# Kernel tuning notes

Hardware: AMD Instinct MI355X
Metric: run time of the kernel (lower is better)

## Reference

```python
import jax, jax.numpy as jnp
import numpy as np

PAD, BOS, EOS, UNK = 0, 1, 2, 3
B, S, V, D, L = 256, 512, 50000, 256, 128

def setup_inputs() -> dict:
    key = jax.random.key(0)
    ks = jax.random.split(key, 12)
    vocab_tensor = jax.random.randint(ks[0], (B, S), 4, V)
    parent_idx = jax.random.randint(ks[1], (B, S), 0, S)
    pbond = jax.random.randint(ks[2], (B, S), 0, 4)
    bond = jax.random.randint(ks[3], (B, S), 0, 4)
    patom = jax.random.randint(ks[4], (B, S), 0, 16)
    atom = jax.random.randint(ks[5], (B, S), 0, 16)
    btype = jax.random.randint(ks[6], (B, S), 0, 4)
    order_tensor = jnp.stack([parent_idx, pbond, bond, patom, atom, btype], axis=-1)
    lengths = jax.random.randint(ks[7], (B,), 1, S + 1)
    mask_tensor = jnp.arange(S)[None, :] < lengths[:, None]  # ragged prefix masks
    eps = jax.random.normal(ks[8], (B, L), dtype=jnp.float32)
    sc = 1.0 / np.sqrt(D)
    emb = jax.random.normal(ks[9], (V, D), dtype=jnp.float32) * sc
    Wm = jax.random.normal(ks[10], (D, L), dtype=jnp.float32) * sc
    Wv = jax.random.normal(ks[11], (D, L), dtype=jnp.float32) * sc
    Wlin = jax.random.normal(jax.random.fold_in(key, 20), (L, D), dtype=jnp.float32) / np.sqrt(L)
    Wout = jax.random.normal(jax.random.fold_in(key, 21), (D, D), dtype=jnp.float32) * sc
    return {
        'vocab_tensor': vocab_tensor, 'order_tensor': order_tensor, 'mask_tensor': mask_tensor,
        'eps': eps, 'emb': emb, 'Wm': Wm, 'bm': jnp.zeros((L,), jnp.float32),
        'Wv': Wv, 'bv': jnp.zeros((L,), jnp.float32), 'Wlin': Wlin,
        'blin': jnp.zeros((D,), jnp.float32), 'Wout': Wout, 'bout': jnp.zeros((D,), jnp.float32),
    }

def _forward(vocab_tensor, order_tensor, mask_tensor, eps, emb, Wm, bm, Wv, bv, Wlin, blin, Wout, bout):
    # --- mask bond-pos columns (torch.where assignments, vectorized) ---
    # (columns 1 and 2 set to -1 where masked; kept implicitly via vt/pad handling)
    # --- calc_chem_z path: masked vocab, parent gather, edge one-hot ---
    vt = jnp.where(mask_tensor, vocab_tensor, PAD)                      # [B,S]
    vocab_emb = emb[vt]                                                 # [B,S,D]
    oi = order_tensor[..., 0]
    oi = jnp.where(oi == -1, BOS, oi)
    parent = jnp.where(mask_tensor, jnp.take_along_axis(vt, oi, axis=1), PAD)
    parent = parent.at[:, 0].set(BOS)
    parent_emb = emb[parent]                                            # [B,S,D]
    idx = jnp.clip(order_tensor[..., 5] - 1, -1, None)
    edge_type = jnp.where((idx >= 0)[..., None],
                          jax.nn.one_hot(jnp.clip(idx, 0), 3, dtype=jnp.float32), 0.0)  # [B,S,3]
    # pooling stand-in for (undefined) StructureEncoder -> [B,D]
    m = mask_tensor[..., None].astype(jnp.float32)
    enc = ((vocab_emb + parent_emb) * m).sum(1) / jnp.maximum(m.sum(1), 1.0)
    enc = enc * (1.0 + 0.0 * edge_type.sum())  # keep edge_type in graph
    # --- LatentSampler ---
    mean = enc @ Wm + bm
    log_var = enc @ Wv + bv
    z = mean + eps * jnp.exp(0.5 * log_var)
    memory = z @ Wlin + blin                                            # [B,D]
    # --- vectorized bos/eos/pad sequence assembly (the hot loop in torch) ---
    inp = jnp.concatenate([jnp.full((B, 1), BOS, vocab_tensor.dtype), vocab_tensor], axis=1)  # [B,S+1]
    mask_ex = jnp.concatenate([jnp.ones((B, 1), bool), mask_tensor], axis=1)
    tgt = jnp.roll(inp, -1, axis=1)
    first_false = jnp.argmax(~mask_ex, axis=1)                          # first eos position
    has_false = jnp.any(~mask_ex, axis=1)
    pos = jnp.arange(S + 1)[None, :]
    tgt = jnp.where(has_false[:, None] & (pos == first_false[:, None] - 1), EOS, tgt)
    kill = has_false[:, None] & (pos >= first_false[:, None])
    tgt = jnp.where(kill, PAD, tgt)
    inp = jnp.where(kill, PAD, inp)
    # edge_index assembly (faithful, consumed by decoder in original)
    padneg = jnp.full((B, 1), -1, order_tensor.dtype)
    edge_index = jnp.concatenate([padneg, jnp.where(mask_tensor, order_tensor[..., 0], -2) + 1], axis=1)
    # --- embedding lookups + decoder stand-in + output head ---
    node_embed = emb[inp]                                               # [B,S+1,D]
    dec = node_embed + memory[:, None, :]
    dec = dec + 0.0 * edge_index[..., None].astype(jnp.float32)         # keep edge_index in graph
    word_emb = dec @ Wout + bout
    tgt_emb = emb[tgt]
    valid = (tgt != PAD)
    sq = (word_emb - tgt_emb) ** 2 * valid[..., None]
    token_loss = sq.sum() / jnp.maximum(valid.sum() * D, 1).astype(jnp.float32)
    kl = -0.5 * jnp.sum(1.0 + log_var - mean ** 2 - jnp.exp(log_var)) / B
    return token_loss, kl

def reference(vocab_tensor, order_tensor, mask_tensor, eps, emb, Wm, bm, Wv, bv, Wlin, blin, Wout, bout):
    return _forward(vocab_tensor, order_tensor, mask_tensor, eps, emb, Wm, bm, Wv, bv, Wlin, blin, Wout, bout)
```

## Files before the change

kernel.cpp:

```cpp
#include <hip/hip_runtime.h>

#define B_ 256
#define S_ 512
#define V_ 50000
#define D_ 256
#define L_ 128
#define PGRID 512

typedef __attribute__((ext_vector_type(8))) short short8;
typedef __attribute__((ext_vector_type(4))) float floatx4;

#define OFF_LENS 16
#define OFF_Q    (OFF_LENS + B_)
#define OFF_WT   (OFF_Q + B_ * D_)
#define OFF_SQP  (OFF_WT + 32768)
#define OFF_EB   (OFF_SQP + 256)
#define OFF_P    (OFF_EB + (V_ * D_ / 2))

__device__ __forceinline__ unsigned short f2bf(float x) {
    unsigned u = __float_as_uint(x);
    u += 0x7FFFu + ((u >> 16) & 1u);
    return (unsigned short)(u >> 16);
}
__device__ __forceinline__ float bf2f(unsigned short u) {
    return __uint_as_float(((unsigned)u) << 16);
}

__global__ __launch_bounds__(256) void prep_kernel(const float* __restrict__ emb,
                                                   unsigned short* __restrict__ embb) {
    const int N4 = V_ * D_ / 4;
    for (int i = blockIdx.x * 256 + threadIdx.x; i < N4; i += gridDim.x * 256) {
        float4 v = ((const float4*)emb)[i];
        ushort4 h;
        h.x = f2bf(v.x); h.y = f2bf(v.y); h.z = f2bf(v.z); h.w = f2bf(v.w);
        ((ushort4*)embb)[i] = h;
    }
}

__global__ __launch_bounds__(256) void wt_kernel(const float* __restrict__ Wout,
                                                 unsigned short* __restrict__ Wt,
                                                 float* __restrict__ ws) {
    __shared__ float sT[64][65];
    if (blockIdx.x == 0 && blockIdx.y == 0) {
        int t = threadIdx.x;
        if (t < 16) ((int*)ws)[t] = 0;
        ws[OFF_SQP + t] = 0.f;
    }
    const int k0 = blockIdx.x * 64, n0 = blockIdx.y * 64;
    const int c = threadIdx.x & 63, rg = threadIdx.x >> 6;
#pragma unroll
    for (int i = 0; i < 16; ++i) {
        int r = rg * 16 + i;
        sT[c][r] = Wout[(k0 + r) * D_ + n0 + c];
    }
    __syncthreads();
#pragma unroll
    for (int i = 0; i < 16; ++i) {
        int r = rg * 16 + i;
        Wt[(size_t)(n0 + r) * D_ + k0 + c] = f2bf(sT[r][c]);
    }
}

__global__ __launch_bounds__(1024) void enclat_kernel(
    const int* __restrict__ vocab, const int* __restrict__ order,
    const int* __restrict__ mask, const float* __restrict__ emb,
    const float* __restrict__ eps,
    const float* __restrict__ Wm, const float* __restrict__ bm,
    const float* __restrict__ Wv, const float* __restrict__ bv,
    const float* __restrict__ Wlin, const float* __restrict__ blin,
    const float* __restrict__ Wout, const float* __restrict__ bout,
    int* __restrict__ lens, float* __restrict__ Q, float* __restrict__ kl_acc) {
    __shared__ int s_id1[S_], s_id2[S_];
    __shared__ float4 s_part[15 * 64];
    __shared__ float s_enc[D_];
    __shared__ float s_mean[L_], s_lv[L_], s_z[L_], s_mem[D_];
    __shared__ float s_red[256];
    __shared__ int s_cnt;
    const int b = blockIdx.x;
    const int tid = threadIdx.x;
    if (tid == 0) s_cnt = 0;
    __syncthreads();
    if (tid < S_) {
        int j = tid;
        int mk = mask[b * S_ + j];
        int id1 = 0, id2 = 0;
        if (mk) {
            id1 = vocab[b * S_ + j];
            if (j == 0) {
                id2 = 1;
            } else {
                int oi = order[(size_t)(b * S_ + j) * 6];
                if (oi == -1) oi = 1;
                id2 = mask[b * S_ + oi] ? vocab[b * S_ + oi] : 0;
            }
        }
        s_id1[j] = id1;
        s_id2[j] = id2;
        unsigned long long bal = __ballot(mk != 0);
        if ((tid & 63) == 0) atomicAdd(&s_cnt, __popcll(bal));
    }
    __syncthreads();
    const int cnt = s_cnt;
    if (tid == 0) lens[b] = cnt;
    const int jg = tid >> 6, d4 = tid & 63;
    const float4* emb4 = (const float4*)emb;
    float4 a = {0.f, 0.f, 0.f, 0.f};
#pragma unroll 4
    for (int j = jg; j < cnt; j += 16) {
        float4 x = emb4[(size_t)s_id1[j] * 64 + d4];
        float4 y = emb4[(size_t)s_id2[j] * 64 + d4];
        a.x += x.x + y.x; a.y += x.y + y.y; a.z += x.z + y.z; a.w += x.w + y.w;
    }
    if (jg) s_part[(jg - 1) * 64 + d4] = a;
    __syncthreads();
    if (jg == 0) {
#pragma unroll
        for (int g = 0; g < 15; ++g) {
            float4 p = s_part[g * 64 + d4];
            a.x += p.x; a.y += p.y; a.z += p.z; a.w += p.w;
        }
        float inv = 1.f / fmaxf((float)cnt, 1.f);
        a.x *= inv; a.y *= inv; a.z *= inv; a.w *= inv;
        ((float4*)s_enc)[d4] = a;
    }
    __syncthreads();
    float dot = 0.f;
    if (tid < 256) {
        const int l = tid & (L_ - 1);
        const float* W = (tid < L_) ? Wm : Wv;
        const float* bb = (tid < L_) ? bm : bv;
        dot = bb[l];
        for (int d = 0; d < D_; ++d) dot = fmaf(s_enc[d], W[d * L_ + l], dot);
        if (tid < L_) s_mean[l] = dot; else s_lv[l] = dot;
    }
    __syncthreads();
    float klp = 0.f;
    if (tid < L_) {
        float mn = s_mean[tid], lv = s_lv[tid];
        s_z[tid] = mn + eps[b * L_ + tid] * expf(0.5f * lv);
        klp = 1.f + lv - mn * mn - expf(lv);
    }
    if (tid < 256) s_red[tid] = klp;
    __syncthreads();
    for (int s = 128; s > 0; s >>= 1) {
        if (tid < s) s_red[tid] += s_red[tid + s];
        __syncthreads();
    }
    if (tid == 0) atomicAdd(kl_acc, s_red[0]);
    if (tid < 256) {
        float mem = blin[tid];
        for (int l2 = 0; l2 < L_; ++l2) mem = fmaf(s_z[l2], Wlin[l2 * D_ + tid], mem);
        s_mem[tid] = mem;
    }
    __syncthreads();
    if (tid < 256) {
        float qv = bout[tid];
        for (int k = 0; k < D_; ++k) qv = fmaf(s_mem[k], Wout[k * D_ + tid], qv);
        Q[b * D_ + tid] = qv;
    }
}

__global__ __launch_bounds__(256, 2) void pgemm_kernel(
    const unsigned short* __restrict__ embb, const unsigned short* __restrict__ Wt,
    unsigned short* __restrict__ P) {
    const int tid = threadIdx.x;
    const int wv = tid >> 6, lane = tid & 63;
    const int lo = lane & 15, hi = lane >> 4;
    const int NCH = V_ / 16;

    short8 bfr[4][8];
    const unsigned short* wbase = Wt + (size_t)(wv * 64 + lo) * D_ + hi * 8;
#pragma unroll
    for (int nt = 0; nt < 4; ++nt)
#pragma unroll
        for (int kk = 0; kk < 8; ++kk)
            bfr[nt][kk] = *(const short8*)(wbase + nt * 16 * D_ + kk * 32);

    int ch = blockIdx.x;
    const unsigned short* abase = embb + (size_t)(ch * 16 + lo) * D_ + hi * 8;
    short8 acur[8];
#pragma unroll
    for (int kk = 0; kk < 8; ++kk) acur[kk] = *(const short8*)(abase + kk * 32);

    for (; ch < NCH; ch += PGRID) {
        const int chn = (ch + PGRID < NCH) ? (ch + PGRID) : ch;
        const unsigned short* anext = embb + (size_t)(chn * 16 + lo) * D_ + hi * 8;
        short8 anxt[8];
#pragma unroll
        for (int kk = 0; kk < 8; ++kk) anxt[kk] = *(const short8*)(anext + kk * 32);

        floatx4 acc[4];
#pragma unroll
        for (int nt = 0; nt < 4; ++nt) acc[nt] = (floatx4){0.f, 0.f, 0.f, 0.f};
#pragma unroll
        for (int kk = 0; kk < 8; ++kk)
#pragma unroll
            for (int nt = 0; nt < 4; ++nt)
                acc[nt] = __builtin_amdgcn_mfma_f32_16x16x32_bf16(
                    acur[kk], bfr[nt][kk], acc[nt], 0, 0, 0);

#pragma unroll
        for (int r = 0; r < 4; ++r) {
            unsigned short* prow = P + (size_t)(ch * 16 + hi * 4 + r) * D_ + wv * 64 + lo;
#pragma unroll
            for (int nt = 0; nt < 4; ++nt) prow[nt * 16] = f2bf(acc[nt][r]);
        }
#pragma unroll
        for (int kk = 0; kk < 8; ++kk) acur[kk] = anxt[kk];
    }
}

__global__ __launch_bounds__(256) void scan_kernel(
    const int* __restrict__ vocab, const unsigned short* __restrict__ embb,
    const unsigned short* __restrict__ P, const float* __restrict__ Q,
    const int* __restrict__ lens, float* __restrict__ sqp) {
    const int tid = threadIdx.x;
    const int wv = tid >> 6, lane = tid & 63;
    const int b = blockIdx.y, chunk = blockIdx.x;
    const int len = lens[b];
    const int j0 = chunk * 16 + wv * 4;
    if (j0 > len) return;

    const int c = lane * 4;
    const float4 q4 = *(const float4*)(Q + (size_t)b * D_ + c);
    float acc = 0.f;
#pragma unroll
    for (int jj = 0; jj < 4; ++jj) {
        const int j = j0 + jj;
        if (j > len) break;
        const int inp = (j == 0) ? 1 : vocab[b * S_ + j - 1];
        const int tgt = (j < len) ? vocab[b * S_ + j] : ((len < S_) ? 2 : 1);
        const ushort4 pv = *(const ushort4*)(P + (size_t)inp * D_ + c);
        const ushort4 tv = *(const ushort4*)(embb + (size_t)tgt * D_ + c);
        float d0 = bf2f(pv.x) + q4.x - bf2f(tv.x);
        float d1 = bf2f(pv.y) + q4.y - bf2f(tv.y);
        float d2 = bf2f(pv.z) + q4.z - bf2f(tv.z);
        float d3 = bf2f(pv.w) + q4.w - bf2f(tv.w);
        acc = fmaf(d0, d0, acc);
        acc = fmaf(d1, d1, acc);
        acc = fmaf(d2, d2, acc);
        acc = fmaf(d3, d3, acc);
    }
#pragma unroll
    for (int off = 32; off; off >>= 1) acc += __shfl_down(acc, off, 64);
    if (lane == 0) atomicAdd(&sqp[(blockIdx.y * 4 + wv + blockIdx.x) & 255], acc);
}

__global__ __launch_bounds__(256) void finalize_kernel(const float* __restrict__ ws,
                                                       float* __restrict__ out) {
    __shared__ float s_sq[256];
    __shared__ int s_vc[256];
    const int tid = threadIdx.x;
    s_sq[tid] = ws[OFF_SQP + tid];
    s_vc[tid] = ((const int*)ws)[OFF_LENS + tid] + 1;
    __syncthreads();
    for (int s = 128; s > 0; s >>= 1) {
        if (tid < s) {
            s_sq[tid] += s_sq[tid + s];
            s_vc[tid] += s_vc[tid + s];
        }
        __syncthreads();
    }
    if (tid == 0) {
        long long denom = (long long)s_vc[0] * D_;
        if (denom < 1) denom = 1;
        out[0] = s_sq[0] / (float)denom;
        out[1] = -0.5f * ws[1] / (float)B_;
    }
}

extern "C" void kernel_launch(void* const* d_in, const int* in_sizes, int n_in,
                              void* d_out, int out_size, void* d_ws, size_t ws_size,
                              hipStream_t stream) {
    const int* vocab = (const int*)d_in[0];
    const int* order = (const int*)d_in[1];
    const int* mask  = (const int*)d_in[2];
    const float* eps  = (const float*)d_in[3];
    const float* emb  = (const float*)d_in[4];
    const float* Wm   = (const float*)d_in[5];
    const float* bm   = (const float*)d_in[6];
    const float* Wv   = (const float*)d_in[7];
    const float* bv   = (const float*)d_in[8];
    const float* Wlin = (const float*)d_in[9];
    const float* blin = (const float*)d_in[10];
    const float* Wout = (const float*)d_in[11];
    const float* bout = (const float*)d_in[12];

    float* ws = (float*)d_ws;
    int* lens = (int*)(ws + OFF_LENS);
    float* Q = ws + OFF_Q;
    unsigned short* Wt = (unsigned short*)(ws + OFF_WT);
    float* sqp = ws + OFF_SQP;
    unsigned short* embb = (unsigned short*)(ws + OFF_EB);
    unsigned short* P = (unsigned short*)(ws + OFF_P);

    wt_kernel<<<dim3(4, 4), 256, 0, stream>>>(Wout, Wt, ws);
    prep_kernel<<<2048, 256, 0, stream>>>(emb, embb);
    enclat_kernel<<<B_, 1024, 0, stream>>>(vocab, order, mask, emb, eps, Wm, bm,
                                           Wv, bv, Wlin, blin, Wout, bout,
                                           lens, Q, ws + 1);
    pgemm_kernel<<<PGRID, 256, 0, stream>>>(embb, Wt, P);
    scan_kernel<<<dim3(33, B_), 256, 0, stream>>>(vocab, embb, P, Q, lens, sqp);
    finalize_kernel<<<1, 256, 0, stream>>>(ws, (float*)d_out);
}
```

Before: 201.7 us.

## Fuse Wout transpose into prep, gather bf16 embeddings in encoder, batch scan loads

Merges the Wout transpose/convert kernel into the embedding bf16 conversion kernel, removing one launch. The encoder mean-pool now gathers from the bf16 embedding copy instead of fp32, halving gathered bytes but making the pooled encoder output depend on bf16-rounded embeddings. The scan kernel processes 8 positions per wave with all gather loads issued up front and predicated weights, which raises memory-level parallelism and halves the grid. Rows past the length are now loaded and multiplied by zero rather than skipped.

```diff
diff --git a/kernel.cpp b/kernel.cpp
--- a/kernel.cpp
+++ b/kernel.cpp
@@ -27,9 +27,34 @@
 }
 
 __global__ __launch_bounds__(256) void prep_kernel(const float* __restrict__ emb,
-                                                   unsigned short* __restrict__ embb) {
+                                                   const float* __restrict__ Wout,
+                                                   unsigned short* __restrict__ embb,
+                                                   unsigned short* __restrict__ Wt,
+                                                   float* __restrict__ ws) {
+    __shared__ float sT[64][65];
+    const int tid = threadIdx.x;
+    if (blockIdx.x == 0) {
+        if (tid < 16) ((int*)ws)[tid] = 0;
+        ws[OFF_SQP + tid] = 0.f;
+    }
+    if (blockIdx.x < 16) {
+        const int bx = blockIdx.x;
+        const int k0 = (bx & 3) * 64, n0 = (bx >> 2) * 64;
+        const int c = tid & 63, rg = tid >> 6;
+#pragma unroll
+        for (int i = 0; i < 16; ++i) {
+            int r = rg * 16 + i;
+            sT[c][r] = Wout[(k0 + r) * D_ + n0 + c];
+        }
+        __syncthreads();
+#pragma unroll
+        for (int i = 0; i < 16; ++i) {
+            int r = rg * 16 + i;
+            Wt[(size_t)(n0 + r) * D_ + k0 + c] = f2bf(sT[r][c]);
+        }
+    }
     const int N4 = V_ * D_ / 4;
-    for (int i = blockIdx.x * 256 + threadIdx.x; i < N4; i += gridDim.x * 256) {
+    for (int i = blockIdx.x * 256 + tid; i < N4; i += gridDim.x * 256) {
         float4 v = ((const float4*)emb)[i];
         ushort4 h;
         h.x = f2bf(v.x); h.y = f2bf(v.y); h.z = f2bf(v.z); h.w = f2bf(v.w);
@@ -37,33 +62,9 @@
     }
 }
 
-__global__ __launch_bounds__(256) void wt_kernel(const float* __restrict__ Wout,
-                                                 unsigned short* __restrict__ Wt,
-                                                 float* __restrict__ ws) {
-    __shared__ float sT[64][65];
-    if (blockIdx.x == 0 && blockIdx.y == 0) {
-        int t = threadIdx.x;
-        if (t < 16) ((int*)ws)[t] = 0;
-        ws[OFF_SQP + t] = 0.f;
-    }
-    const int k0 = blockIdx.x * 64, n0 = blockIdx.y * 64;
-    const int c = threadIdx.x & 63, rg = threadIdx.x >> 6;
-#pragma unroll
-    for (int i = 0; i < 16; ++i) {
-        int r = rg * 16 + i;
-        sT[c][r] = Wout[(k0 + r) * D_ + n0 + c];
-    }
-    __syncthreads();
-#pragma unroll
-    for (int i = 0; i < 16; ++i) {
-        int r = rg * 16 + i;
-        Wt[(size_t)(n0 + r) * D_ + k0 + c] = f2bf(sT[r][c]);
-    }
-}
-
 __global__ __launch_bounds__(1024) void enclat_kernel(
     const int* __restrict__ vocab, const int* __restrict__ order,
-    const int* __restrict__ mask, const float* __restrict__ emb,
+    const int* __restrict__ mask, const unsigned short* __restrict__ embb,
     const float* __restrict__ eps,
     const float* __restrict__ Wm, const float* __restrict__ bm,
     const float* __restrict__ Wv, const float* __restrict__ bv,
@@ -103,13 +104,16 @@
     const int cnt = s_cnt;
     if (tid == 0) lens[b] = cnt;
     const int jg = tid >> 6, d4 = tid & 63;
-    const float4* emb4 = (const float4*)emb;
+    const ushort4* eb4 = (const ushort4*)embb;
     float4 a = {0.f, 0.f, 0.f, 0.f};
 #pragma unroll 4
     for (int j = jg; j < cnt; j += 16) {
-        float4 x = emb4[(size_t)s_id1[j] * 64 + d4];
-        float4 y = emb4[(size_t)s_id2[j] * 64 + d4];
-        a.x += x.x + y.x; a.y += x.y + y.y; a.z += x.z + y.z; a.w += x.w + y.w;
+        ushort4 x = eb4[(size_t)s_id1[j] * 64 + d4];
+        ushort4 y = eb4[(size_t)s_id2[j] * 64 + d4];
+        a.x += bf2f(x.x) + bf2f(y.x);
+        a.y += bf2f(x.y) + bf2f(y.y);
+        a.z += bf2f(x.z) + bf2f(y.z);
+        a.w += bf2f(x.w) + bf2f(y.w);
     }
     if (jg) s_part[(jg - 1) * 64 + d4] = a;
     __syncthreads();
@@ -218,32 +222,42 @@
     const int wv = tid >> 6, lane = tid & 63;
     const int b = blockIdx.y, chunk = blockIdx.x;
     const int len = lens[b];
-    const int j0 = chunk * 16 + wv * 4;
+    const int j0 = chunk * 32 + wv * 8;
     if (j0 > len) return;
 
     const int c = lane * 4;
     const float4 q4 = *(const float4*)(Q + (size_t)b * D_ + c);
+
+    int inp[8], tgt[8];
+    float wgt[8];
+#pragma unroll
+    for (int jj = 0; jj < 8; ++jj) {
+        const int j = j0 + jj;
+        const bool v = (j <= len);
+        const int jc = v ? j : 0;
+        inp[jj] = (jc == 0) ? 1 : vocab[b * S_ + jc - 1];
+        tgt[jj] = v ? ((j < len) ? vocab[b * S_ + j] : ((len < S_) ? 2 : 1)) : 1;
+        wgt[jj] = v ? 1.f : 0.f;
+    }
+    ushort4 pv[8], tv[8];
+#pragma unroll
+    for (int jj = 0; jj < 8; ++jj) {
+        pv[jj] = *(const ushort4*)(P + (size_t)inp[jj] * D_ + c);
+        tv[jj] = *(const ushort4*)(embb + (size_t)tgt[jj] * D_ + c);
+    }
     float acc = 0.f;
 #pragma unroll
-    for (int jj = 0; jj < 4; ++jj) {
-        const int j = j0 + jj;
-        if (j > len) break;
-        const int inp = (j == 0) ? 1 : vocab[b * S_ + j - 1];
-        const int tgt = (j < len) ? vocab[b * S_ + j] : ((len < S_) ? 2 : 1);
-        const ushort4 pv = *(const ushort4*)(P + (size_t)inp * D_ + c);
-        const ushort4 tv = *(const ushort4*)(embb + (size_t)tgt * D_ + c);
-        float d0 = bf2f(pv.x) + q4.x - bf2f(tv.x);
-        float d1 = bf2f(pv.y) + q4.y - bf2f(tv.y);
-        float d2 = bf2f(pv.z) + q4.z - bf2f(tv.z);
-        float d3 = bf2f(pv.w) + q4.w - bf2f(tv.w);
-        acc = fmaf(d0, d0, acc);
-        acc = fmaf(d1, d1, acc);
-        acc = fmaf(d2, d2, acc);
-        acc = fmaf(d3, d3, acc);
+    for (int jj = 0; jj < 8; ++jj) {
+        float d0 = bf2f(pv[jj].x) + q4.x - bf2f(tv[jj].x);
+        float d1 = bf2f(pv[jj].y) + q4.y - bf2f(tv[jj].y);
+        float d2 = bf2f(pv[jj].z) + q4.z - bf2f(tv[jj].z);
+        float d3 = bf2f(pv[jj].w) + q4.w - bf2f(tv[jj].w);
+        float s = fmaf(d0, d0, fmaf(d1, d1, fmaf(d2, d2, d3 * d3)));
+        acc = fmaf(wgt[jj], s, acc);
     }
 #pragma unroll
     for (int off = 32; off; off >>= 1) acc += __shfl_down(acc, off, 64);
-    if (lane == 0) atomicAdd(&sqp[(blockIdx.y * 4 + wv + blockIdx.x) & 255], acc);
+    if (lane == 0) atomicAdd(&sqp[(b * 4 + wv + chunk) & 255], acc);
 }
 
 __global__ __launch_bounds__(256) void finalize_kernel(const float* __restrict__ ws,
@@ -294,12 +308,11 @@
     unsigned short* embb = (unsigned short*)(ws + OFF_EB);
     unsigned short* P = (unsigned short*)(ws + OFF_P);
 
-    wt_kernel<<<dim3(4, 4), 256, 0, stream>>>(Wout, Wt, ws);
-    prep_kernel<<<2048, 256, 0, stream>>>(emb, embb);
-    enclat_kernel<<<B_, 1024, 0, stream>>>(vocab, order, mask, emb, eps, Wm, bm,
+    prep_kernel<<<2048, 256, 0, stream>>>(emb, Wout, embb, Wt, ws);
+    enclat_kernel<<<B_, 1024, 0, stream>>>(vocab, order, mask, embb, eps, Wm, bm,
                                            Wv, bv, Wlin, blin, Wout, bout,
                                            lens, Q, ws + 1);
     pgemm_kernel<<<PGRID, 256, 0, stream>>>(embb, Wt, P);
-    scan_kernel<<<dim3(33, B_), 256, 0, stream>>>(vocab, embb, P, Q, lens, sqp);
+    scan_kernel<<<dim3(17, B_), 256, 0, stream>>>(vocab, embb, P, Q, lens, sqp);
     finalize_kernel<<<1, 256, 0, stream>>>(ws, (float*)d_out);
 }
```

Result: faster. 181.6 us (-10.0%).
